# Kernel optimization log

Measured on AMD Instinct MI355X. Metric: run time of the kernel, lower is better.

Reference implementation:

```python
import jax, jax.numpy as jnp
import numpy as np

H = 16            # num_heads
SEG = 2048        # segment_size
DIL = 8           # dilation_rate
BLOCK_M = 64      # triton query block size (min(64, M_padded))


def setup_inputs() -> dict:
    key = jax.random.key(0)
    k1, k2, k3 = jax.random.split(key, 3)
    B, M, D = 2, 8192, 1024
    x = jax.random.normal(k1, (B, M, D), dtype=jnp.float32)
    Wqkv = jax.random.normal(k2, (3 * D, D), dtype=jnp.float32) * 0.02
    Wout = jax.random.normal(k3, (D, D), dtype=jnp.float32) * 0.02
    return {"x": x, "Wqkv": Wqkv, "Wout": Wout}


def reference(x, Wqkv, Wout):
    B, M, D = x.shape
    hd = D // H
    scale = hd ** -0.5
    S = M // SEG                      # number of segments (M is a multiple of SEG)
    Kn = SEG // DIL                   # dilated keys per segment
    nb = SEG // BLOCK_M               # query blocks per segment

    # qkv projection (torch Linear: x @ W^T), split into q,k,v: [B,H,M,hd]
    qkv = jnp.einsum('bmd,ed->bme', x, Wqkv).reshape(B, M, 3, H, hd)
    qkv = jnp.transpose(qkv, (2, 0, 3, 1, 4))
    q, k, v = qkv[0] * scale, qkv[1], qkv[2]

    # segment-local views
    q4 = q.reshape(B, H, S, SEG, hd)
    k4 = k.reshape(B, H, S, SEG, hd)[:, :, :, ::DIL]   # [B,H,S,Kn,hd] dilated keys
    v4 = v.reshape(B, H, S, SEG, hd)[:, :, :, ::DIL]

    # scores per segment: [B,H,S,SEG,Kn]
    scores = jnp.einsum('bhspd,bhskd->bhspk', q4, k4)
    # kernel normalization: per key j, subtract max over the 64-query block
    scores = scores.reshape(B, H, S, nb, BLOCK_M, Kn)
    c = jnp.max(scores, axis=4, keepdims=True)          # [B,H,S,nb,1,Kn]
    w = jnp.exp(scores - c)
    den = jnp.sum(w, axis=-1) + 1e-10                   # [B,H,S,nb,BLOCK_M]
    num = jnp.einsum('bhsnmk,bhskd->bhsnmd', w, v4)
    out = num / den[..., None]                          # [B,H,S,nb,BLOCK_M,hd]

    out = out.reshape(B, H, M, hd)
    out = jnp.transpose(out, (0, 2, 1, 3)).reshape(B, M, D)
    return jnp.einsum('bmd,ed->bme', out, Wout)
```

## Files before the change

kernel.cpp:

```cpp
#include <hip/hip_runtime.h>
#include <hip/hip_bf16.h>
#include <stdint.h>


typedef __attribute__((ext_vector_type(8))) short short8;
typedef __attribute__((ext_vector_type(4))) float f32x4;
typedef __attribute__((ext_vector_type(4))) unsigned short ushort4v;

#define DEVI static __device__ __forceinline__

DEVI unsigned short f2bf(float f) {
  union { float f; uint32_t u; } v; v.f = f;
  return (unsigned short)((v.u + 0x7FFFu + ((v.u >> 16) & 1u)) >> 16);
}

DEVI uint32_t pack_bf16(float lo, float hi) {
  return (uint32_t)f2bf(lo) | ((uint32_t)f2bf(hi) << 16);
}

DEVI void gload_lds16(const void* g, void* l) {
  __builtin_amdgcn_global_load_lds((const __attribute__((address_space(1))) void*)g,
                                   (__attribute__((address_space(3))) void*)l,
                                   16, 0, 0);
}

__global__ void cvt_kernel(const float* __restrict__ in, unsigned short* __restrict__ out, int n) {
  int i = (blockIdx.x * 256 + threadIdx.x) * 4;
  if (i >= n) return;
  float4 f = *(const float4*)(in + i);
  uint2 o;
  o.x = (uint32_t)f2bf(f.x) | ((uint32_t)f2bf(f.y) << 16);
  o.y = (uint32_t)f2bf(f.z) | ((uint32_t)f2bf(f.w) << 16);
  *(uint2*)(out + i) = o;
}

template<int EPI>
__global__ __launch_bounds__(256, 2) void gemm_bt(
    const unsigned short* __restrict__ A, const unsigned short* __restrict__ B,
    void* __restrict__ Cv, unsigned short* __restrict__ Cv2,
    float scale, long a_row_stride, int ldc, int K)
{
  __shared__ unsigned short smA[128 * 64];
  __shared__ unsigned short smB[128 * 64];
  const int tid = threadIdx.x;
  const int tm = blockIdx.x, tn = blockIdx.y;
  const int w = tid >> 6, lane = tid & 63;
  const int wr = (w >> 1) * 64, wc = (w & 1) * 64;
  const int lr = lane & 15, lq = lane >> 4;

  int se[4], srow[4], scol[4];
#pragma unroll
  for (int i = 0; i < 4; ++i) {
    int e = (i * 256 + tid) * 8;
    int r = e >> 6;
    int cc = (e >> 3) & 7;
    se[i] = e; srow[i] = r; scol[i] = (cc ^ (r & 7)) * 8;
  }

  f32x4 acc[4][4] = {};

  for (int kt = 0; kt < K / 64; ++kt) {
    if (kt) __syncthreads();
#pragma unroll
    for (int i = 0; i < 4; ++i)
      gload_lds16(A + (long)(tm * 128 + srow[i]) * a_row_stride + kt * 64 + scol[i], &smA[se[i]]);
#pragma unroll
    for (int i = 0; i < 4; ++i)
      gload_lds16(B + (long)(tn * 128 + srow[i]) * K + kt * 64 + scol[i], &smB[se[i]]);
    __syncthreads();

#pragma unroll
    for (int kk = 0; kk < 2; ++kk) {
      int kc = kk * 4 + lq;
      short8 af[4], bfm[4];
#pragma unroll
      for (int i = 0; i < 4; ++i) {
        int row = wr + i * 16 + lr;
        af[i] = *(const short8*)&smA[row * 64 + ((kc ^ (row & 7)) * 8)];
      }
#pragma unroll
      for (int j = 0; j < 4; ++j) {
        int row = wc + j * 16 + lr;
        bfm[j] = *(const short8*)&smB[row * 64 + ((kc ^ (row & 7)) * 8)];
      }
#pragma unroll
      for (int i = 0; i < 4; ++i)
#pragma unroll
        for (int j = 0; j < 4; ++j)
          acc[i][j] = __builtin_amdgcn_mfma_f32_16x16x32_bf16(af[i], bfm[j], acc[i][j], 0, 0, 0);
    }
  }

  if (EPI == 2 && tn >= 8) {
    const int fbase = (tn - 8) * 128 + wc;
#pragma unroll
    for (int ip = 0; ip < 4; ip += 2) {
      int t0 = tm * 128 + wr + ip * 16 + lq * 4;
      int seg = t0 >> 8;
      int ts  = t0 & 255;
      int c32 = (ts >> 5) * 16 + (ts & 15);
#pragma unroll
      for (int j = 0; j < 4; ++j) {
        int f = fbase + j * 16 + lr;
        uint32_t* rp = (uint32_t*)&Cv2[((long)(seg * 1024 + f)) * 256];
        uint4 U;
        U.x = pack_bf16(acc[ip][j][0] * scale, acc[ip + 1][j][0] * scale);
        U.y = pack_bf16(acc[ip][j][1] * scale, acc[ip + 1][j][1] * scale);
        U.z = pack_bf16(acc[ip][j][2] * scale, acc[ip + 1][j][2] * scale);
        U.w = pack_bf16(acc[ip][j][3] * scale, acc[ip + 1][j][3] * scale);
        *(uint4*)&rp[c32] = U;
      }
    }
    return;
  }

#pragma unroll
  for (int i = 0; i < 4; ++i) {
    int rg0 = tm * 128 + wr + i * 16 + lq * 4;
#pragma unroll
    for (int j = 0; j < 4; ++j) {
      int cg = tn * 128 + wc + j * 16 + lr;
#pragma unroll
      for (int r = 0; r < 4; ++r) {
        float v = acc[i][j][r] * scale;
        long off = (long)(rg0 + r) * ldc + cg;
        if (EPI == 0) ((float*)Cv)[off] = v;
        else          ((unsigned short*)Cv)[off] = f2bf(v);
      }
    }
  }
}

__global__ __launch_bounds__(256, 3) void attn_kernel(
    const unsigned short* __restrict__ qb,
    const unsigned short* __restrict__ kb,
    const unsigned short* __restrict__ vtb,
    unsigned short* __restrict__ attout)
{
  __shared__ unsigned short v_t[64 * 256];
  __shared__ uint32_t w32[64 * 68];

  const int u = (blockIdx.x & 7) * 128 + (blockIdx.x >> 3);
  const int e8 = u & 7, h = (u >> 3) & 15, s = (u >> 7) & 3, b = u >> 9;
  const int tid = threadIdx.x, w = tid >> 6, lane = tid & 63;
  const int lr = lane & 15, lq = lane >> 4;
  const long qrow0 = (long)b * 8192 + s * 2048 + e8 * 256;
  const int hc = h * 64;

  const unsigned short* kbase = kb + ((long)(b * 4 + s) * 256) * 1024 + hc;
  const unsigned short* vbase = vtb + ((long)(b * 4 + s) * 1024 + hc) * 256;

#pragma unroll
  for (int it = 0; it < 8; ++it) {
    int e = (it * 256 + tid) * 8;
    int f = e >> 8;
    int ch = (e >> 3) & 31;
    gload_lds16(vbase + (long)f * 256 + ((ch ^ (f & 7)) * 8), &v_t[e]);
  }

  short8 bk[2][2][2];
#pragma unroll
  for (int half = 0; half < 2; ++half)
#pragma unroll
    for (int kk = 0; kk < 2; ++kk)
#pragma unroll
      for (int jf = 0; jf < 2; ++jf)
        bk[half][kk][jf] = *(const short8*)
          &kbase[(long)(half * 128 + w * 32 + jf * 16 + lr) * 1024 + (kk * 4 + lq) * 8];

  __syncthreads();

  short8 ones;
#pragma unroll
  for (int e = 0; e < 8; ++e) ones[e] = (short)0x3F80;

  for (int qblk = 0; qblk < 4; ++qblk) {
    const unsigned short* qbase = qb + (qrow0 + qblk * 64) * 1024 + hc;
    f32x4 acc_pv[4] = {};
    f32x4 acc_den = {};

#pragma unroll
    for (int half = 0; half < 2; ++half) {
      f32x4 acc_s[4][2] = {};
#pragma unroll
      for (int kk = 0; kk < 2; ++kk) {
        int kc = kk * 4 + lq;
        short8 aq[4];
#pragma unroll
        for (int i = 0; i < 4; ++i)
          aq[i] = *(const short8*)&qbase[(i * 16 + lr) * 1024 + kc * 8];
#pragma unroll
        for (int i = 0; i < 4; ++i)
#pragma unroll
          for (int j = 0; j < 2; ++j)
            acc_s[i][j] = __builtin_amdgcn_mfma_f32_16x16x32_bf16(aq[i], bk[half][kk][j], acc_s[i][j], 0, 0, 0);
      }

      float cmax[2];
#pragma unroll
      for (int j = 0; j < 2; ++j) {
        float m = -3.4e38f;
#pragma unroll
        for (int i = 0; i < 4; ++i)
#pragma unroll
          for (int r = 0; r < 4; ++r) m = fmaxf(m, acc_s[i][j][r]);
        m = fmaxf(m, __shfl_xor(m, 16));
        m = fmaxf(m, __shfl_xor(m, 32));
        cmax[j] = m;
      }

#pragma unroll
      for (int i = 0; i < 4; ++i) {
#pragma unroll
        for (int r = 0; r < 4; ++r) {
          int q = i * 16 + lq * 4 + r;
          uint32_t pk = pack_bf16(__expf(acc_s[i][0][r] - cmax[0]),
                                  __expf(acc_s[i][1][r] - cmax[1]));
          w32[q * 68 + w * 16 + lr] = pk;
        }
      }
      __syncthreads();

#pragma unroll
      for (int ks = 0; ks < 4; ++ks) {
        int kc = ks * 4 + lq;
        short8 bw = *(const short8*)&w32[(w * 16 + lr) * 68 + kc * 4];
        acc_den = __builtin_amdgcn_mfma_f32_16x16x32_bf16(ones, bw, acc_den, 0, 0, 0);
#pragma unroll
        for (int ct = 0; ct < 4; ++ct) {
          int frow = ct * 16 + lr;
          short8 av = *(const short8*)&v_t[frow * 256 + (((half * 16 + kc) ^ (lr & 7)) << 3)];
          acc_pv[ct] = __builtin_amdgcn_mfma_f32_16x16x32_bf16(av, bw, acc_pv[ct], 0, 0, 0);
        }
      }
      __syncthreads();
    }

    float inv = 1.0f / (acc_den[0] + 1e-10f);
    long orow = (qrow0 + qblk * 64 + w * 16 + lr) * 1024 + hc;
#pragma unroll
    for (int ct = 0; ct < 4; ++ct) {
      ushort4v p;
#pragma unroll
      for (int r = 0; r < 4; ++r) p[r] = f2bf(acc_pv[ct][r] * inv);
      *(ushort4v*)&attout[orow + ct * 16 + lq * 4] = p;
    }
  }
}

extern "C" void kernel_launch(void* const* d_in, const int* in_sizes, int n_in,
                              void* d_out, int out_size, void* d_ws, size_t ws_size,
                              hipStream_t stream) {
  (void)in_sizes; (void)n_in; (void)out_size; (void)ws_size;
  const float* x    = (const float*)d_in[0];
  const float* Wqkv = (const float*)d_in[1];
  const float* Wout = (const float*)d_in[2];
  float* out = (float*)d_out;
  char* ws = (char*)d_ws;

  unsigned short* xb     = (unsigned short*)(ws);
  unsigned short* attout = (unsigned short*)(ws);
  unsigned short* wqkvb  = (unsigned short*)(ws + 33554432);
  unsigned short* woutb  = (unsigned short*)(ws + 39845888);
  unsigned short* qbuf   = (unsigned short*)(ws + 41943040);
  unsigned short* kbuf   = (unsigned short*)(ws + 75497472);
  unsigned short* vtb    = (unsigned short*)(ws + 79691776);

  cvt_kernel<<<16384, 256, 0, stream>>>(x, xb, 16777216);
  cvt_kernel<<<3072, 256, 0, stream>>>(Wqkv, wqkvb, 3 * 1024 * 1024);
  cvt_kernel<<<1024, 256, 0, stream>>>(Wout, woutb, 1024 * 1024);

  gemm_bt<1><<<dim3(128, 8), 256, 0, stream>>>(
      xb, wqkvb, (void*)qbuf, nullptr, 0.125f, 1024, 1024, 1024);
  gemm_bt<2><<<dim3(16, 16), 256, 0, stream>>>(
      xb, wqkvb + 1024 * 1024, (void*)kbuf, vtb, 1.0f, 8192, 1024, 1024);

  attn_kernel<<<1024, 256, 0, stream>>>(qbuf, kbuf, vtb, attout);

  gemm_bt<0><<<dim3(128, 8), 256, 0, stream>>>(
      attout, woutb, (void*)out, nullptr, 1.0f, 1024, 1024, 1024);
}
```

Before: 198.2 us.

## Give each wave its own query block and stream keys through per-wave chunks

The attention kernel now assigns each of the four waves its own 64-query block. Before, the four waves split the keys of one block and exchanged exp weights through shared LDS with block-wide barriers. Each wave keeps its Q fragments in registers, loops over 8 key chunks of 32 keys, prefetches the next chunk's K from global memory, and writes weights to a private LDS slice, so the per-chunk __syncthreads calls go away. The cost is more accumulator registers (16 PV tiles plus 4 denominators), so launch bounds drop from 3 to 2 blocks per CU, which may reduce occupancy.

```diff
diff --git a/kernel.cpp b/kernel.cpp
--- a/kernel.cpp
+++ b/kernel.cpp
@@ -131,20 +131,20 @@
   }
 }
 
-__global__ __launch_bounds__(256, 3) void attn_kernel(
+__global__ __launch_bounds__(256, 2) void attn_kernel(
     const unsigned short* __restrict__ qb,
     const unsigned short* __restrict__ kb,
     const unsigned short* __restrict__ vtb,
     unsigned short* __restrict__ attout)
 {
   __shared__ unsigned short v_t[64 * 256];
-  __shared__ uint32_t w32[64 * 68];
+  __shared__ uint32_t w32[4][64][18];
 
   const int u = (blockIdx.x & 7) * 128 + (blockIdx.x >> 3);
   const int e8 = u & 7, h = (u >> 3) & 15, s = (u >> 7) & 3, b = u >> 9;
   const int tid = threadIdx.x, w = tid >> 6, lane = tid & 63;
   const int lr = lane & 15, lq = lane >> 4;
-  const long qrow0 = (long)b * 8192 + s * 2048 + e8 * 256;
+  const long qrow0 = (long)b * 8192 + s * 2048 + e8 * 256 + w * 64;
   const int hc = h * 64;
 
   const unsigned short* kbase = kb + ((long)(b * 4 + s) * 256) * 1024 + hc;
@@ -158,15 +158,13 @@
     gload_lds16(vbase + (long)f * 256 + ((ch ^ (f & 7)) * 8), &v_t[e]);
   }
 
-  short8 bk[2][2][2];
-#pragma unroll
-  for (int half = 0; half < 2; ++half)
+  const unsigned short* qbase = qb + qrow0 * 1024 + hc;
+  short8 aq[4][2];
+#pragma unroll
+  for (int i = 0; i < 4; ++i)
 #pragma unroll
     for (int kk = 0; kk < 2; ++kk)
-#pragma unroll
-      for (int jf = 0; jf < 2; ++jf)
-        bk[half][kk][jf] = *(const short8*)
-          &kbase[(long)(half * 128 + w * 32 + jf * 16 + lr) * 1024 + (kk * 4 + lq) * 8];
+      aq[i][kk] = *(const short8*)&qbase[(i * 16 + lr) * 1024 + (kk * 4 + lq) * 8];
 
   __syncthreads();
 
@@ -174,75 +172,92 @@
 #pragma unroll
   for (int e = 0; e < 8; ++e) ones[e] = (short)0x3F80;
 
-  for (int qblk = 0; qblk < 4; ++qblk) {
-    const unsigned short* qbase = qb + (qrow0 + qblk * 64) * 1024 + hc;
-    f32x4 acc_pv[4] = {};
-    f32x4 acc_den = {};
-
-#pragma unroll
-    for (int half = 0; half < 2; ++half) {
-      f32x4 acc_s[4][2] = {};
-#pragma unroll
-      for (int kk = 0; kk < 2; ++kk) {
-        int kc = kk * 4 + lq;
-        short8 aq[4];
-#pragma unroll
-        for (int i = 0; i < 4; ++i)
-          aq[i] = *(const short8*)&qbase[(i * 16 + lr) * 1024 + kc * 8];
-#pragma unroll
-        for (int i = 0; i < 4; ++i)
-#pragma unroll
-          for (int j = 0; j < 2; ++j)
-            acc_s[i][j] = __builtin_amdgcn_mfma_f32_16x16x32_bf16(aq[i], bk[half][kk][j], acc_s[i][j], 0, 0, 0);
-      }
-
-      float cmax[2];
-#pragma unroll
-      for (int j = 0; j < 2; ++j) {
-        float m = -3.4e38f;
-#pragma unroll
-        for (int i = 0; i < 4; ++i)
-#pragma unroll
-          for (int r = 0; r < 4; ++r) m = fmaxf(m, acc_s[i][j][r]);
-        m = fmaxf(m, __shfl_xor(m, 16));
-        m = fmaxf(m, __shfl_xor(m, 32));
-        cmax[j] = m;
-      }
-
-#pragma unroll
-      for (int i = 0; i < 4; ++i) {
-#pragma unroll
-        for (int r = 0; r < 4; ++r) {
-          int q = i * 16 + lq * 4 + r;
-          uint32_t pk = pack_bf16(__expf(acc_s[i][0][r] - cmax[0]),
-                                  __expf(acc_s[i][1][r] - cmax[1]));
-          w32[q * 68 + w * 16 + lr] = pk;
-        }
-      }
-      __syncthreads();
-
-#pragma unroll
-      for (int ks = 0; ks < 4; ++ks) {
-        int kc = ks * 4 + lq;
-        short8 bw = *(const short8*)&w32[(w * 16 + lr) * 68 + kc * 4];
-        acc_den = __builtin_amdgcn_mfma_f32_16x16x32_bf16(ones, bw, acc_den, 0, 0, 0);
-#pragma unroll
-        for (int ct = 0; ct < 4; ++ct) {
-          int frow = ct * 16 + lr;
-          short8 av = *(const short8*)&v_t[frow * 256 + (((half * 16 + kc) ^ (lr & 7)) << 3)];
-          acc_pv[ct] = __builtin_amdgcn_mfma_f32_16x16x32_bf16(av, bw, acc_pv[ct], 0, 0, 0);
-        }
-      }
-      __syncthreads();
-    }
-
-    float inv = 1.0f / (acc_den[0] + 1e-10f);
-    long orow = (qrow0 + qblk * 64 + w * 16 + lr) * 1024 + hc;
+  uint32_t (*wsl)[18] = w32[w];
+
+  f32x4 acc_pv[4][4] = {};
+  f32x4 acc_den[4] = {};
+
+  short8 bkc[2][2], bkn[2][2];
+#pragma unroll
+  for (int j = 0; j < 2; ++j)
+#pragma unroll
+    for (int kk = 0; kk < 2; ++kk)
+      bkc[j][kk] = *(const short8*)&kbase[(long)(j * 16 + lr) * 1024 + (kk * 4 + lq) * 8];
+
+#pragma unroll
+  for (int c = 0; c < 8; ++c) {
+    if (c < 7) {
+#pragma unroll
+      for (int j = 0; j < 2; ++j)
+#pragma unroll
+        for (int kk = 0; kk < 2; ++kk)
+          bkn[j][kk] = *(const short8*)
+            &kbase[(long)((c + 1) * 32 + j * 16 + lr) * 1024 + (kk * 4 + lq) * 8];
+    }
+
+    f32x4 acc_s[4][2] = {};
+#pragma unroll
+    for (int kk = 0; kk < 2; ++kk)
+#pragma unroll
+      for (int i = 0; i < 4; ++i)
+#pragma unroll
+        for (int j = 0; j < 2; ++j)
+          acc_s[i][j] = __builtin_amdgcn_mfma_f32_16x16x32_bf16(aq[i][kk], bkc[j][kk], acc_s[i][j], 0, 0, 0);
+
+    float cmax[2];
+#pragma unroll
+    for (int j = 0; j < 2; ++j) {
+      float m = -3.4e38f;
+#pragma unroll
+      for (int i = 0; i < 4; ++i)
+#pragma unroll
+        for (int r = 0; r < 4; ++r) m = fmaxf(m, acc_s[i][j][r]);
+      m = fmaxf(m, __shfl_xor(m, 16));
+      m = fmaxf(m, __shfl_xor(m, 32));
+      cmax[j] = m;
+    }
+
+#pragma unroll
+    for (int i = 0; i < 4; ++i) {
+#pragma unroll
+      for (int r = 0; r < 4; ++r) {
+        int q = i * 16 + lq * 4 + r;
+        wsl[q][lr] = pack_bf16(__expf(acc_s[i][0][r] - cmax[0]),
+                               __expf(acc_s[i][1][r] - cmax[1]));
+      }
+    }
+
+    short8 av[4];
+#pragma unroll
+    for (int ct = 0; ct < 4; ++ct) {
+      int frow = ct * 16 + lr;
+      av[ct] = *(const short8*)&v_t[frow * 256 + (((c * 4 + lq) ^ (frow & 7)) << 3)];
+    }
+#pragma unroll
+    for (int qi = 0; qi < 4; ++qi) {
+      short8 bw = *(const short8*)&wsl[qi * 16 + lr][lq * 4];
+      acc_den[qi] = __builtin_amdgcn_mfma_f32_16x16x32_bf16(ones, bw, acc_den[qi], 0, 0, 0);
+#pragma unroll
+      for (int ct = 0; ct < 4; ++ct)
+        acc_pv[qi][ct] = __builtin_amdgcn_mfma_f32_16x16x32_bf16(av[ct], bw, acc_pv[qi][ct], 0, 0, 0);
+    }
+
+#pragma unroll
+    for (int j = 0; j < 2; ++j)
+#pragma unroll
+      for (int kk = 0; kk < 2; ++kk)
+        bkc[j][kk] = bkn[j][kk];
+  }
+
+#pragma unroll
+  for (int qi = 0; qi < 4; ++qi) {
+    float inv = 1.0f / (acc_den[qi][0] + 1e-10f);
+    long orow = (qrow0 + qi * 16 + lr) * 1024 + hc;
 #pragma unroll
     for (int ct = 0; ct < 4; ++ct) {
       ushort4v p;
 #pragma unroll
-      for (int r = 0; r < 4; ++r) p[r] = f2bf(acc_pv[ct][r] * inv);
+      for (int r = 0; r < 4; ++r) p[r] = f2bf(acc_pv[qi][ct][r] * inv);
       *(ushort4v*)&attout[orow + ct * 16 + lq * 4] = p;
     }
   }
```

After: 184.1 us. 7.1% less time.
